# Performance work log

Hardware: AMD Instinct MI355X
Metric: run time of the kernel (lower is better)

The kernel has to match this reference:

```python
import jax, jax.numpy as jnp
import numpy as np

B, R, S, L, H, A, TD = 4, 8, 8, 256, 768, 256, 100


def setup_inputs() -> dict:
    key = jax.random.key(0)
    ks = iter(jax.random.split(key, 64))
    n = lambda *s: jax.random.normal(next(ks), s, jnp.float32)
    p = lambda *s: jax.random.normal(next(ks), s, jnp.float32) * 0.02
    inp = {
        'X': n(B, L, H),
        'X_mean': n(B, H),
        'mask': jnp.ones((B, L), jnp.float32),
        'sk': jax.random.randint(next(ks), (B, R, S, 2), 0, L, dtype=jnp.int32),
        'sk_mask': jnp.ones((B, R, S), jnp.float32),
        'semantic_rel_emb': n(R, H),
        'transe_rel_emb': n(R, TD),
    }
    # 4 EntityExtractors (reconstructed as two H->1 linears producing start/end logits)
    for pref in ('fh', 'bt', 'ft', 'bh'):
        inp[pref + '_ws'] = p(H); inp[pref + '_bs'] = p()
        inp[pref + '_we'] = p(H); inp[pref + '_be'] = p()
    # 2 RelationAttentions (fwd: rel_dim=H, bwd: rel_dim=TD)
    for pref, rd in (('fra', H), ('bra', TD)):
        inp[pref + '_Wx'] = p(H, A);  inp[pref + '_bx'] = p(A)
        inp[pref + '_Wr'] = p(rd, A); inp[pref + '_br'] = p(A)
        inp[pref + '_Wg'] = p(H, A);  inp[pref + '_bg'] = p(A)
        inp[pref + '_V'] = p(A);      inp[pref + '_bv'] = p()
    # 2 FuseExtractors
    for pref in ('ffe', 'bfe'):
        inp[pref + '_Ws'] = p(H, H); inp[pref + '_bs'] = p(H)
        inp[pref + '_Wx'] = p(H, H); inp[pref + '_bx'] = p(H)
    return inp


def _entity(h, ws, bs, we, be):
    # EntityExtractor: start/end logits over last (H) axis
    return jnp.einsum('...h,h->...', h, ws) + bs, jnp.einsum('...h,h->...', h, we) + be


def _rel_attn(X, rel, g, Wx, bx, Wr, br, Wg, bg, V, bv):
    wx = X @ Wx + bx          # (B,L,A)
    wr = rel @ Wr + br        # (R,A)
    wg = g @ Wg + bg          # (B,A)
    z = jnp.tanh(wx[:, None, :, :] + wr[None, :, None, :] + wg[:, None, None, :])  # (B,R,L,A)
    e = jnp.einsum('brla,a->brl', z, V) + bv
    a = jax.nn.softmax(e, axis=-1)                       # (B,R,L)
    c = jnp.einsum('brl,blh->brh', a, X)                 # (B,R,H)
    return c, a


def _sk_to_embeddings(sk, sk_mask, X):
    # vectorized span-endpoint gather + average (replaces B*R*S python loop)
    b_idx = jnp.arange(X.shape[0])[:, None, None]        # (B,1,1)
    emb = (X[b_idx, sk[..., 0]] + X[b_idx, sk[..., 1]]) * 0.5   # (B,R,S,H)
    return sk_mask[..., None] * emb


def _fuse(X, c, sk_embs, sk_mask, Ws, bs, Wx, bx):
    w_x = X @ Wx + bx                                    # (B,L,H)
    w_sk = (sk_embs @ Ws + bs) * sk_mask[..., None]      # (B,R,S,H)
    # h_ijk = Ws*sk + Wx*x_i + c_j + x_i  -> (B,R,S,L,H)
    return (w_sk[:, :, :, None, :] + w_x[:, None, None, :, :]
            + c[:, :, None, None, :] + X[:, None, None, :, :])


def reference(X, X_mean, mask, sk, sk_mask, semantic_rel_emb, transe_rel_emb,
              fh_ws, fh_bs, fh_we, fh_be, bt_ws, bt_bs, bt_we, bt_be,
              ft_ws, ft_bs, ft_we, ft_be, bh_ws, bh_bs, bh_we, bh_be,
              fra_Wx, fra_bx, fra_Wr, fra_br, fra_Wg, fra_bg, fra_V, fra_bv,
              bra_Wx, bra_bx, bra_Wr, bra_br, bra_Wg, bra_bg, bra_V, bra_bv,
              ffe_Ws, ffe_bs, ffe_Wx, ffe_bx, bfe_Ws, bfe_bs, bfe_Wx, bfe_bx):
    fh_s, fh_e = _entity(X, fh_ws, fh_bs, fh_we, fh_be)      # (B,L)
    bt_s, bt_e = _entity(X, bt_ws, bt_bs, bt_we, bt_be)      # (B,L)
    fwd_c, _ = _rel_attn(X, semantic_rel_emb, X_mean,
                         fra_Wx, fra_bx, fra_Wr, fra_br, fra_Wg, fra_bg, fra_V, fra_bv)
    bwd_c, _ = _rel_attn(X, transe_rel_emb, X_mean,
                         bra_Wx, bra_bx, bra_Wr, bra_br, bra_Wg, bra_bg, bra_V, bra_bv)
    sk_embs = _sk_to_embeddings(sk, sk_mask, X)              # (B,R,S,H)
    fwd_hijk = _fuse(X, fwd_c, sk_embs, sk_mask, ffe_Ws, ffe_bs, ffe_Wx, ffe_bx)
    bwd_hijk = _fuse(X, bwd_c, sk_embs, sk_mask, bfe_Ws, bfe_bs, bfe_Wx, bfe_bx)
    ft_s, ft_e = _entity(fwd_hijk, ft_ws, ft_bs, ft_we, ft_be)  # (B,R,S,L)
    bh_s, bh_e = _entity(bwd_hijk, bh_ws, bh_bs, bh_we, bh_be)  # (B,R,S,L)
    return (fh_s, fh_e, bt_s, bt_e, ft_s, ft_e, bh_s, bh_e)
```

## Files before the change

### kernel.cpp

```cpp
#include <hip/hip_runtime.h>
#include <hip/hip_bf16.h>

#define NB 4
#define NR 8
#define NS 8
#define NL 256
#define NH 768
#define NA 256
#define NTD 100

#define WX_F 0
#define WX_B (WX_F + NB*NL*NA)
#define WR_F (WX_B + NB*NL*NA)
#define WR_B (WR_F + NR*NA)
#define WG_F (WR_B + NR*NA)
#define WG_B (WG_F + NB*NA)
#define C_F  (WG_B + NB*NA)
#define C_B  (C_F + NB*NR*NH)
#define QV   (C_B + NB*NR*NH)
#define SCAL (QV + 8*NH)
#define DXL  (SCAL + 8)
#define XB   (DXL + 4*NB*NL)
#define WT   (XB + (NB*NL*NH)/2)

#define O_FT_S 4096
#define O_FT_E 69632
#define O_BH_S 135168
#define O_BH_E 200704

typedef __attribute__((ext_vector_type(8))) short short8;
typedef __attribute__((ext_vector_type(4))) float f32x4;

struct bh4 { __hip_bfloat16 a, b, c, d; };

__device__ __forceinline__ float tanh_fast(float x) {
    x = fminf(15.f, fmaxf(-15.f, x));
    float t = __expf(2.f * x);
    return (t - 1.f) / (t + 1.f);
}

__device__ __forceinline__ float wave_reduce(float v) {
    #pragma unroll
    for (int off = 32; off > 0; off >>= 1) v += __shfl_down(v, off);
    return v;
}

__global__ void __launch_bounds__(512) k_setup(const float* __restrict__ X,
                      const float* __restrict__ fra_Wx, const float* __restrict__ bra_Wx,
                      const float* __restrict__ sem, const float* __restrict__ transe,
                      const float* __restrict__ X_mean,
                      const float* __restrict__ fra_Wr, const float* __restrict__ fra_br,
                      const float* __restrict__ fra_Wg, const float* __restrict__ fra_bg,
                      const float* __restrict__ bra_Wr, const float* __restrict__ bra_br,
                      const float* __restrict__ bra_Wg, const float* __restrict__ bra_bg,
                      const float* __restrict__ ffe_Ws, const float* __restrict__ ffe_bs,
                      const float* __restrict__ ffe_Wx, const float* __restrict__ ffe_bx,
                      const float* __restrict__ bfe_Ws, const float* __restrict__ bfe_bs,
                      const float* __restrict__ bfe_Wx, const float* __restrict__ bfe_bx,
                      const float* __restrict__ ft_ws, const float* __restrict__ ft_we,
                      const float* __restrict__ bh_ws, const float* __restrict__ bh_we,
                      float* __restrict__ ws) {
    __shared__ float smem[2112];
    const int bid = blockIdx.x, tid = threadIdx.x;

    if (bid < 384) {
        __hip_bfloat16* xb = (__hip_bfloat16*)(ws + XB);
        const int i0 = bid*2048 + tid*4;
        const float4 v = *(const float4*)(X + i0);
        bh4 o = { __float2bfloat16(v.x), __float2bfloat16(v.y),
                  __float2bfloat16(v.z), __float2bfloat16(v.w) };
        *(bh4*)(xb + i0) = o;
    } else if (bid < 576) {
        __hip_bfloat16* wt = (__hip_bfloat16*)(ws + WT);
        const int t2 = bid - 384;
        const int mt = t2 / 96;
        const int half = tid >> 8, tid2 = tid & 255;
        const int tile = (t2 % 96)*2 + half;
        const int h0 = (tile >> 3) * 32, c0 = (tile & 7) * 32;
        const float* W = mt ? bra_Wx : fra_Wx;
        float (*sh)[33] = (float(*)[33])(smem + half*1056);
        const int r = tid2 >> 5, c = tid2 & 31;
        #pragma unroll
        for (int i = 0; i < 4; ++i)
            sh[r + 8*i][c] = W[(size_t)(h0 + r + 8*i)*NA + c0 + c];
        __syncthreads();
        const int cw = tid2 >> 5, hw = tid2 & 31;
        #pragma unroll
        for (int i = 0; i < 4; ++i)
            wt[(size_t)(mt*NA + c0 + cw + 8*i)*NH + h0 + hw] = __float2bfloat16(sh[hw][cw + 8*i]);
    } else if (bid < 600) {
        float* sh = smem;
        float* red2 = smem + 768;
        const int q = bid - 576;
        const float* s; const float* W; const float* bias; float* out; int K;
        if (q < 8)       { s = sem + q*NH;         W = fra_Wr; bias = fra_br; out = ws + WR_F + q*NA;      K = NH;  }
        else if (q < 16) { s = transe + (q-8)*NTD; W = bra_Wr; bias = bra_br; out = ws + WR_B + (q-8)*NA;  K = NTD; }
        else if (q < 20) { s = X_mean + (q-16)*NH; W = fra_Wg; bias = fra_bg; out = ws + WG_F + (q-16)*NA; K = NH;  }
        else             { s = X_mean + (q-20)*NH; W = bra_Wg; bias = bra_bg; out = ws + WG_B + (q-20)*NA; K = NH;  }
        for (int j = tid; j < K; j += 512) sh[j] = s[j];
        __syncthreads();
        const int half = tid >> 8, col = tid & 255;
        const int khalf = (K/2) & ~15;
        const int k0 = half ? khalf : 0, k1 = half ? K : khalf;
        const float* Wc = W + col;
        float acc = 0.f;
        int k = k0;
        for (; k + 16 <= k1; k += 16) {
            float wb[16];
            #pragma unroll
            for (int i = 0; i < 16; ++i) wb[i] = Wc[(size_t)(k+i)*NA];
            #pragma unroll
            for (int i = 0; i < 16; ++i) acc += sh[k+i] * wb[i];
        }
        for (; k < k1; ++k) acc += sh[k] * Wc[(size_t)k*NA];
        red2[half*256 + col] = acc;
        __syncthreads();
        if (half == 0) out[col] = red2[col] + red2[256 + col] + bias[col];
    } else if (bid < 608) {
        float* red2 = smem;
        const int q = bid - 600;
        const float* a; const float* b2;
        switch (q) {
            case 0: a = ffe_bs; b2 = ft_ws; break;
            case 1: a = ffe_bs; b2 = ft_we; break;
            case 2: a = ffe_bx; b2 = ft_ws; break;
            case 3: a = ffe_bx; b2 = ft_we; break;
            case 4: a = bfe_bs; b2 = bh_ws; break;
            case 5: a = bfe_bs; b2 = bh_we; break;
            case 6: a = bfe_bx; b2 = bh_ws; break;
            default: a = bfe_bx; b2 = bh_we; break;
        }
        float p = a[tid]*b2[tid];
        if (tid < 256) p += a[tid+512]*b2[tid+512];
        red2[tid] = p; __syncthreads();
        for (int s2 = 256; s2 > 0; s2 >>= 1) { if (tid < s2) red2[tid] += red2[tid + s2]; __syncthreads(); }
        if (tid == 0) ws[SCAL + q] = red2[0];
    } else {
        const int idx = bid - 608;
        const int mi = idx / 96;
        const int row = (idx % 96)*8 + (tid >> 6);
        const int lane = tid & 63;
        const float* M; const float* v0; const float* v1; bool self;
        switch (mi) {
            case 0: M = ffe_Ws; v0 = ft_ws; v1 = ft_we; self = false; break;
            case 1: M = bfe_Ws; v0 = bh_ws; v1 = bh_we; self = false; break;
            case 2: M = ffe_Wx; v0 = ft_ws; v1 = ft_we; self = true;  break;
            default: M = bfe_Wx; v0 = bh_ws; v1 = bh_we; self = true; break;
        }
        const float4* mr4 = (const float4*)(M + (size_t)row*NH);
        const float4* va4 = (const float4*)v0;
        const float4* vb4 = (const float4*)v1;
        float a0 = 0.f, a1 = 0.f;
        #pragma unroll
        for (int i = 0; i < 3; ++i) {
            const float4 m4 = mr4[lane + 64*i];
            const float4 x4 = va4[lane + 64*i];
            const float4 y4 = vb4[lane + 64*i];
            a0 += m4.x*x4.x + m4.y*x4.y + m4.z*x4.z + m4.w*x4.w;
            a1 += m4.x*y4.x + m4.y*y4.y + m4.z*y4.z + m4.w*y4.w;
        }
        a0 = wave_reduce(a0); a1 = wave_reduce(a1);
        if (lane == 0) {
            ws[QV + (mi*2 + 0)*NH + row] = a0 + (self ? v0[row] : 0.f);
            ws[QV + (mi*2 + 1)*NH + row] = a1 + (self ? v1[row] : 0.f);
        }
    }
}

__global__ void __launch_bounds__(256) k_wx(const float* __restrict__ fra_bx,
                                            const float* __restrict__ bra_bx,
                                            float* __restrict__ ws) {
    const __hip_bfloat16* xb = (const __hip_bfloat16*)(ws + XB);
    const __hip_bfloat16* wt = (const __hip_bfloat16*)(ws + WT);
    const int bid = blockIdx.x, tid = threadIdx.x;
    const int fb = bid >> 8;
    const int rt = (bid & 255) >> 2, cg = bid & 3;
    const int wv = tid >> 6, lane = tid & 63;
    const int m0 = rt * 16, c0 = cg * 64 + wv * 16;
    const int r16 = lane & 15, koff = (lane >> 4) * 8;

    const short8* ap = (const short8*)(xb + (size_t)(m0 + r16)*NH + koff);
    const short8* bp = (const short8*)(wt + (size_t)(fb*NA + c0 + r16)*NH + koff);

    f32x4 acc = {0.f, 0.f, 0.f, 0.f};
    #pragma unroll
    for (int ks = 0; ks < 24; ks += 4) {
        short8 a0 = ap[(ks+0)*4], b0 = bp[(ks+0)*4];
        short8 a1 = ap[(ks+1)*4], b1 = bp[(ks+1)*4];
        short8 a2 = ap[(ks+2)*4], b2 = bp[(ks+2)*4];
        short8 a3 = ap[(ks+3)*4], b3 = bp[(ks+3)*4];
        acc = __builtin_amdgcn_mfma_f32_16x16x32_bf16(a0, b0, acc, 0, 0, 0);
        acc = __builtin_amdgcn_mfma_f32_16x16x32_bf16(a1, b1, acc, 0, 0, 0);
        acc = __builtin_amdgcn_mfma_f32_16x16x32_bf16(a2, b2, acc, 0, 0, 0);
        acc = __builtin_amdgcn_mfma_f32_16x16x32_bf16(a3, b3, acc, 0, 0, 0);
    }
    const float* bia = fb ? bra_bx : fra_bx;
    float* outp = ws + (fb ? WX_B : WX_F);
    const int col = c0 + r16;
    const float bb = bia[col];
    const int rbase = m0 + (lane >> 4) * 4;
    #pragma unroll
    for (int j = 0; j < 4; ++j)
        outp[(size_t)(rbase + j)*NA + col] = acc[j] + bb;
}

__global__ void __launch_bounds__(512) k_attn_dxl(const float* __restrict__ X,
                       const float* __restrict__ fra_V, const float* __restrict__ fra_bv,
                       const float* __restrict__ bra_V, const float* __restrict__ bra_bv,
                       const float* __restrict__ fh_ws, const float* __restrict__ fh_bs,
                       const float* __restrict__ fh_we, const float* __restrict__ fh_be,
                       const float* __restrict__ bt_ws, const float* __restrict__ bt_bs,
                       const float* __restrict__ bt_we, const float* __restrict__ bt_be,
                       float* __restrict__ ws, float* __restrict__ out) {
    __shared__ float smem[1536];
    const int bid = blockIdx.x, tid = threadIdx.x;

    if (bid < 64) {
        float* wa_s = smem;
        float* v_s  = smem + 256;
        float* red  = smem + 512;
        float* part = smem + 768;
        float* a_s  = smem + 1024;
        const int fb = bid >> 5, b = (bid >> 3) & 3, r = bid & 7;
        const int l = tid & 255, half = tid >> 8;

        const float* wr = ws + (fb ? WR_B : WR_F) + r*NA;
        const float* wg = ws + (fb ? WG_B : WG_F) + b*NA;
        const float* V  = fb ? bra_V : fra_V;
        const float  bv = fb ? bra_bv[0] : fra_bv[0];
        const float* wxp = ws + (fb ? WX_B : WX_F);

        if (tid < 256) { wa_s[tid] = wr[tid] + wg[tid]; v_s[tid] = V[tid]; }
        __syncthreads();

        const float4* wxrow = (const float4*)(wxp + (size_t)(b*NL + l)*NA + half*128);
        float acc = 0.f;
        for (int a0 = 0; a0 < 32; a0 += 8) {
            float4 wb[8];
            #pragma unroll
            for (int i = 0; i < 8; ++i) wb[i] = wxrow[a0 + i];
            #pragma unroll
            for (int i = 0; i < 8; ++i) {
                const int a = half*128 + (a0 + i)*4;
                acc += tanh_fast(wb[i].x + wa_s[a+0]) * v_s[a+0];
                acc += tanh_fast(wb[i].y + wa_s[a+1]) * v_s[a+1];
                acc += tanh_fast(wb[i].z + wa_s[a+2]) * v_s[a+2];
                acc += tanh_fast(wb[i].w + wa_s[a+3]) * v_s[a+3];
            }
        }
        if (half) part[l] = acc;
        __syncthreads();

        float e = 0.f;
        if (!half) e = acc + part[l] + bv;
        if (tid < 256) red[tid] = e;
        __syncthreads();
        for (int s2 = 128; s2 > 0; s2 >>= 1) { if (tid < s2) red[tid] = fmaxf(red[tid], red[tid+s2]); __syncthreads(); }
        const float mx = red[0];
        __syncthreads();
        float p = 0.f;
        if (tid < 256) { p = __expf(e - mx); red[tid] = p; }
        __syncthreads();
        for (int s2 = 128; s2 > 0; s2 >>= 1) { if (tid < s2) red[tid] += red[tid+s2]; __syncthreads(); }
        if (tid < 256) a_s[tid] = p / red[0];
        __syncthreads();

        const float* Xb = X + (size_t)b*NL*NH;
        float* cc = ws + (fb ? C_B : C_F) + (size_t)(b*NR + r)*NH;
        for (int h = tid; h < NH; h += 512) {
            const float* Xp = Xb + h;
            float c = 0.f;
            for (int l0 = 0; l0 < NL; l0 += 8) {
                float xb_[8];
                #pragma unroll
                for (int i = 0; i < 8; ++i) xb_[i] = Xp[(size_t)(l0+i)*NH];
                #pragma unroll
                for (int i = 0; i < 8; ++i) c += a_s[l0+i] * xb_[i];
            }
            cc[h] = c;
        }
    } else {
        float* xr = smem;
        const int idx = bid - 64;
        const int m0 = idx * 2;
        const int g = tid >> 6, lane = tid & 63;
        const int row = g >> 2, w = g & 3;
        const int m = m0 + row;

        if (tid < 384) ((float4*)xr)[tid] = ((const float4*)(X + (size_t)m0*NH))[tid];
        __syncthreads();

        const float* v0; const float* v1; float add0, add1; float* o0; float* o1;
        if (w == 0)      { v0 = fh_ws; add0 = fh_bs[0]; o0 = out;        v1 = fh_we; add1 = fh_be[0]; o1 = out + 1024; }
        else if (w == 1) { v0 = bt_ws; add0 = bt_bs[0]; o0 = out + 2048; v1 = bt_we; add1 = bt_be[0]; o1 = out + 3072; }
        else if (w == 2) { v0 = ws + QV + 4*NH; add0 = ws[SCAL+2]; o0 = ws + DXL;
                           v1 = ws + QV + 5*NH; add1 = ws[SCAL+3]; o1 = ws + DXL + 1024; }
        else             { v0 = ws + QV + 6*NH; add0 = ws[SCAL+6]; o0 = ws + DXL + 2048;
                           v1 = ws + QV + 7*NH; add1 = ws[SCAL+7]; o1 = ws + DXL + 3072; }

        const float4* xr4 = (const float4*)(xr + row*NH);
        const float4* v04 = (const float4*)v0;
        const float4* v14 = (const float4*)v1;
        float a0 = 0.f, a1 = 0.f;
        #pragma unroll
        for (int i = 0; i < 3; ++i) {
            const float4 x4 = xr4[lane + 64*i];
            const float4 p4 = v04[lane + 64*i];
            const float4 q4 = v14[lane + 64*i];
            a0 += x4.x*p4.x + x4.y*p4.y + x4.z*p4.z + x4.w*p4.w;
            a1 += x4.x*q4.x + x4.y*q4.y + x4.z*q4.z + x4.w*q4.w;
        }
        a0 = wave_reduce(a0); a1 = wave_reduce(a1);
        if (lane == 0) { o0[m] = a0 + add0; o1[m] = a1 + add1; }
    }
}

__global__ void __launch_bounds__(256) k_skf(const float* __restrict__ X, const int* __restrict__ sk,
                     const float* __restrict__ sk_mask,
                     const float* __restrict__ ft_ws, const float* __restrict__ ft_bs,
                     const float* __restrict__ ft_we, const float* __restrict__ ft_be,
                     const float* __restrict__ bh_ws, const float* __restrict__ bh_bs,
                     const float* __restrict__ bh_we, const float* __restrict__ bh_be,
                     const float* __restrict__ ws, float* __restrict__ out) {
    __shared__ float avg[NH];
    __shared__ float d1_s[4], d3_s[4];
    const int brs = blockIdx.x;
    const int tid = threadIdx.x, w = tid >> 6, lane = tid & 63;
    const int b = brs >> 6, br = brs >> 3;
    const int i0 = sk[brs*2], i1 = sk[brs*2 + 1];
    const float mk = sk_mask[brs];

    if (tid < 192) {
        const float4 x0 = ((const float4*)(X + (size_t)(b*NL + i0)*NH))[tid];
        const float4 x1 = ((const float4*)(X + (size_t)(b*NL + i1)*NH))[tid];
        float4 o; o.x = 0.5f*(x0.x+x1.x); o.y = 0.5f*(x0.y+x1.y);
        o.z = 0.5f*(x0.z+x1.z); o.w = 0.5f*(x0.w+x1.w);
        ((float4*)avg)[tid] = o;
    }
    __syncthreads();

    const float4* q4 = (const float4*)(ws + QV + w*NH);
    const float4* av4 = (const float4*)avg;
    const float4* c4 = (const float4*)(ws + ((w < 2) ? C_F : C_B) + (size_t)br*NH);
    const float* v = (w == 0) ? ft_ws : (w == 1) ? ft_we : (w == 2) ? bh_ws : bh_we;
    const float4* vv4 = (const float4*)v;
    float acc = 0.f, d = 0.f;
    #pragma unroll
    for (int i = 0; i < 3; ++i) {
        const float4 a4 = av4[lane + 64*i];
        const float4 b4 = q4[lane + 64*i];
        const float4 e4 = c4[lane + 64*i];
        const float4 f4 = vv4[lane + 64*i];
        acc += a4.x*b4.x + a4.y*b4.y + a4.z*b4.z + a4.w*b4.w;
        d   += e4.x*f4.x + e4.y*f4.y + e4.z*f4.z + e4.w*f4.w;
    }
    acc = wave_reduce(acc); d = wave_reduce(d);
    if (lane == 0) {
        const float bsdot = ws[SCAL + ((w < 2) ? w : (w + 2))];
        d1_s[w] = mk*mk*acc + mk*bsdot;
        d3_s[w] = d;
    }
    __syncthreads();

    const int l = tid, m = b*NL + l, o = brs*NL + l;
    out[O_FT_S + o] = d1_s[0] + ws[DXL + 0*1024 + m] + d3_s[0] + ft_bs[0];
    out[O_FT_E + o] = d1_s[1] + ws[DXL + 1*1024 + m] + d3_s[1] + ft_be[0];
    out[O_BH_S + o] = d1_s[2] + ws[DXL + 2*1024 + m] + d3_s[2] + bh_bs[0];
    out[O_BH_E + o] = d1_s[3] + ws[DXL + 3*1024 + m] + d3_s[3] + bh_be[0];
}

extern "C" void kernel_launch(void* const* d_in, const int* in_sizes, int n_in,
                              void* d_out, int out_size, void* d_ws, size_t ws_size,
                              hipStream_t stream) {
    const float* X        = (const float*)d_in[0];
    const float* X_mean   = (const float*)d_in[1];
    const int*   sk       = (const int*)d_in[3];
    const float* sk_mask  = (const float*)d_in[4];
    const float* sem      = (const float*)d_in[5];
    const float* transe   = (const float*)d_in[6];
    const float* fh_ws = (const float*)d_in[7],  *fh_bs = (const float*)d_in[8];
    const float* fh_we = (const float*)d_in[9],  *fh_be = (const float*)d_in[10];
    const float* bt_ws = (const float*)d_in[11], *bt_bs = (const float*)d_in[12];
    const float* bt_we = (const float*)d_in[13], *bt_be = (const float*)d_in[14];
    const float* ft_ws = (const float*)d_in[15], *ft_bs = (const float*)d_in[16];
    const float* ft_we = (const float*)d_in[17], *ft_be = (const float*)d_in[18];
    const float* bh_ws = (const float*)d_in[19], *bh_bs = (const float*)d_in[20];
    const float* bh_we = (const float*)d_in[21], *bh_be = (const float*)d_in[22];
    const float* fra_Wx = (const float*)d_in[23], *fra_bx = (const float*)d_in[24];
    const float* fra_Wr = (const float*)d_in[25], *fra_br = (const float*)d_in[26];
    const float* fra_Wg = (const float*)d_in[27], *fra_bg = (const float*)d_in[28];
    const float* fra_V  = (const float*)d_in[29], *fra_bv = (const float*)d_in[30];
    const float* bra_Wx = (const float*)d_in[31], *bra_bx = (const float*)d_in[32];
    const float* bra_Wr = (const float*)d_in[33], *bra_br = (const float*)d_in[34];
    const float* bra_Wg = (const float*)d_in[35], *bra_bg = (const float*)d_in[36];
    const float* bra_V  = (const float*)d_in[37], *bra_bv = (const float*)d_in[38];
    const float* ffe_Ws = (const float*)d_in[39], *ffe_bs = (const float*)d_in[40];
    const float* ffe_Wx = (const float*)d_in[41], *ffe_bx = (const float*)d_in[42];
    const float* bfe_Ws = (const float*)d_in[43], *bfe_bs = (const float*)d_in[44];
    const float* bfe_Wx = (const float*)d_in[45], *bfe_bx = (const float*)d_in[46];

    float* out = (float*)d_out;
    float* ws  = (float*)d_ws;

    k_setup<<<dim3(992), dim3(512), 0, stream>>>(X, fra_Wx, bra_Wx, sem, transe, X_mean,
        fra_Wr, fra_br, fra_Wg, fra_bg, bra_Wr, bra_br, bra_Wg, bra_bg,
        ffe_Ws, ffe_bs, ffe_Wx, ffe_bx, bfe_Ws, bfe_bs, bfe_Wx, bfe_bx,
        ft_ws, ft_we, bh_ws, bh_we, ws);

    k_wx<<<dim3(512), dim3(256), 0, stream>>>(fra_bx, bra_bx, ws);

    k_attn_dxl<<<dim3(576), dim3(512), 0, stream>>>(X, fra_V, fra_bv, bra_V, bra_bv,
        fh_ws, fh_bs, fh_we, fh_be, bt_ws, bt_bs, bt_we, bt_be, ws, out);

    k_skf<<<dim3(256), dim3(256), 0, stream>>>(X, sk, sk_mask,
        ft_ws, ft_bs, ft_we, ft_be, bh_ws, bh_bs, bh_we, bh_be, ws, out);
}
```

Baseline: 251.2 us.

## Compute attention context with bf16 MFMA over transposed X, split attention kernel

The attention kernel now writes softmax weights as bf16, zero-padded to 16 rows, into a workspace buffer. A new k_ctx kernel computes the context vectors c = a·X with 16x16x32 bf16 MFMA, using a bf16 transposed copy of X that extra setup blocks produce. This replaces the old per-thread strided fp32 loop over L. The row-dot products over X move into their own k_dxl launch with one block per row. The change trades fp32 precision in the context sum and two extra launches for matrix-core throughput and coalesced access.

```diff
diff --git a/kernel.cpp b/kernel.cpp
--- a/kernel.cpp
+++ b/kernel.cpp
@@ -20,8 +20,10 @@
 #define QV   (C_B + NB*NR*NH)
 #define SCAL (QV + 8*NH)
 #define DXL  (SCAL + 8)
-#define XB   (DXL + 4*NB*NL)
+#define ATT16 (DXL + 4*NB*NL)
+#define XB   (ATT16 + 16384)
 #define WT   (XB + (NB*NL*NH)/2)
+#define XT   (WT + (2*NA*NH)/2)
 
 #define O_FT_S 4096
 #define O_FT_E 69632
@@ -84,14 +86,29 @@
         for (int i = 0; i < 4; ++i)
             sh[r + 8*i][c] = W[(size_t)(h0 + r + 8*i)*NA + c0 + c];
         __syncthreads();
-        const int cw = tid2 >> 5, hw = tid2 & 31;
         #pragma unroll
         for (int i = 0; i < 4; ++i)
-            wt[(size_t)(mt*NA + c0 + cw + 8*i)*NH + h0 + hw] = __float2bfloat16(sh[hw][cw + 8*i]);
-    } else if (bid < 600) {
+            wt[(size_t)(mt*NA + c0 + r + 8*i)*NH + h0 + c] = __float2bfloat16(sh[c][r + 8*i]);
+    } else if (bid < 960) {
+        __hip_bfloat16* xt = (__hip_bfloat16*)(ws + XT);
+        const int t2 = bid - 576;
+        const int half = tid >> 8, tid2 = tid & 255;
+        const int tile = t2*2 + half;
+        const int b = tile / 192, trem = tile % 192;
+        const int h0 = (trem >> 3) * 32, l0 = (trem & 7) * 32;
+        float (*sh)[33] = (float(*)[33])(smem + half*1056);
+        const int r = tid2 >> 5, c = tid2 & 31;
+        #pragma unroll
+        for (int i = 0; i < 4; ++i)
+            sh[r + 8*i][c] = X[(size_t)(b*NL + l0 + r + 8*i)*NH + h0 + c];
+        __syncthreads();
+        #pragma unroll
+        for (int i = 0; i < 4; ++i)
+            xt[(size_t)(b*NH + h0 + r + 8*i)*NL + l0 + c] = __float2bfloat16(sh[c][r + 8*i]);
+    } else if (bid < 984) {
         float* sh = smem;
         float* red2 = smem + 768;
-        const int q = bid - 576;
+        const int q = bid - 960;
         const float* s; const float* W; const float* bias; float* out; int K;
         if (q < 8)       { s = sem + q*NH;         W = fra_Wr; bias = fra_br; out = ws + WR_F + q*NA;      K = NH;  }
         else if (q < 16) { s = transe + (q-8)*NTD; W = bra_Wr; bias = bra_br; out = ws + WR_B + (q-8)*NA;  K = NTD; }
@@ -116,9 +133,9 @@
         red2[half*256 + col] = acc;
         __syncthreads();
         if (half == 0) out[col] = red2[col] + red2[256 + col] + bias[col];
-    } else if (bid < 608) {
+    } else if (bid < 992) {
         float* red2 = smem;
-        const int q = bid - 600;
+        const int q = bid - 984;
         const float* a; const float* b2;
         switch (q) {
             case 0: a = ffe_bs; b2 = ft_ws; break;
@@ -136,7 +153,7 @@
         for (int s2 = 256; s2 > 0; s2 >>= 1) { if (tid < s2) red2[tid] += red2[tid + s2]; __syncthreads(); }
         if (tid == 0) ws[SCAL + q] = red2[0];
     } else {
-        const int idx = bid - 608;
+        const int idx = bid - 992;
         const int mi = idx / 96;
         const int row = (idx % 96)*8 + (tid >> 6);
         const int lane = tid & 63;
@@ -204,115 +221,125 @@
         outp[(size_t)(rbase + j)*NA + col] = acc[j] + bb;
 }
 
-__global__ void __launch_bounds__(512) k_attn_dxl(const float* __restrict__ X,
-                       const float* __restrict__ fra_V, const float* __restrict__ fra_bv,
+__global__ void __launch_bounds__(512) k_attn(const float* __restrict__ fra_V, const float* __restrict__ fra_bv,
                        const float* __restrict__ bra_V, const float* __restrict__ bra_bv,
-                       const float* __restrict__ fh_ws, const float* __restrict__ fh_bs,
-                       const float* __restrict__ fh_we, const float* __restrict__ fh_be,
-                       const float* __restrict__ bt_ws, const float* __restrict__ bt_bs,
-                       const float* __restrict__ bt_we, const float* __restrict__ bt_be,
-                       float* __restrict__ ws, float* __restrict__ out) {
-    __shared__ float smem[1536];
+                       float* __restrict__ ws) {
+    __shared__ float wa_s[NA], v_s[NA], red[NL], part[NL];
     const int bid = blockIdx.x, tid = threadIdx.x;
-
-    if (bid < 64) {
-        float* wa_s = smem;
-        float* v_s  = smem + 256;
-        float* red  = smem + 512;
-        float* part = smem + 768;
-        float* a_s  = smem + 1024;
-        const int fb = bid >> 5, b = (bid >> 3) & 3, r = bid & 7;
-        const int l = tid & 255, half = tid >> 8;
-
-        const float* wr = ws + (fb ? WR_B : WR_F) + r*NA;
-        const float* wg = ws + (fb ? WG_B : WG_F) + b*NA;
-        const float* V  = fb ? bra_V : fra_V;
-        const float  bv = fb ? bra_bv[0] : fra_bv[0];
-        const float* wxp = ws + (fb ? WX_B : WX_F);
-
-        if (tid < 256) { wa_s[tid] = wr[tid] + wg[tid]; v_s[tid] = V[tid]; }
-        __syncthreads();
-
-        const float4* wxrow = (const float4*)(wxp + (size_t)(b*NL + l)*NA + half*128);
-        float acc = 0.f;
-        for (int a0 = 0; a0 < 32; a0 += 8) {
-            float4 wb[8];
-            #pragma unroll
-            for (int i = 0; i < 8; ++i) wb[i] = wxrow[a0 + i];
-            #pragma unroll
-            for (int i = 0; i < 8; ++i) {
-                const int a = half*128 + (a0 + i)*4;
-                acc += tanh_fast(wb[i].x + wa_s[a+0]) * v_s[a+0];
-                acc += tanh_fast(wb[i].y + wa_s[a+1]) * v_s[a+1];
-                acc += tanh_fast(wb[i].z + wa_s[a+2]) * v_s[a+2];
-                acc += tanh_fast(wb[i].w + wa_s[a+3]) * v_s[a+3];
-            }
-        }
-        if (half) part[l] = acc;
-        __syncthreads();
-
-        float e = 0.f;
-        if (!half) e = acc + part[l] + bv;
-        if (tid < 256) red[tid] = e;
-        __syncthreads();
-        for (int s2 = 128; s2 > 0; s2 >>= 1) { if (tid < s2) red[tid] = fmaxf(red[tid], red[tid+s2]); __syncthreads(); }
-        const float mx = red[0];
-        __syncthreads();
-        float p = 0.f;
-        if (tid < 256) { p = __expf(e - mx); red[tid] = p; }
-        __syncthreads();
-        for (int s2 = 128; s2 > 0; s2 >>= 1) { if (tid < s2) red[tid] += red[tid+s2]; __syncthreads(); }
-        if (tid < 256) a_s[tid] = p / red[0];
-        __syncthreads();
-
-        const float* Xb = X + (size_t)b*NL*NH;
-        float* cc = ws + (fb ? C_B : C_F) + (size_t)(b*NR + r)*NH;
-        for (int h = tid; h < NH; h += 512) {
-            const float* Xp = Xb + h;
-            float c = 0.f;
-            for (int l0 = 0; l0 < NL; l0 += 8) {
-                float xb_[8];
-                #pragma unroll
-                for (int i = 0; i < 8; ++i) xb_[i] = Xp[(size_t)(l0+i)*NH];
-                #pragma unroll
-                for (int i = 0; i < 8; ++i) c += a_s[l0+i] * xb_[i];
-            }
-            cc[h] = c;
-        }
-    } else {
-        float* xr = smem;
-        const int idx = bid - 64;
-        const int m0 = idx * 2;
-        const int g = tid >> 6, lane = tid & 63;
-        const int row = g >> 2, w = g & 3;
-        const int m = m0 + row;
-
-        if (tid < 384) ((float4*)xr)[tid] = ((const float4*)(X + (size_t)m0*NH))[tid];
-        __syncthreads();
-
-        const float* v0; const float* v1; float add0, add1; float* o0; float* o1;
-        if (w == 0)      { v0 = fh_ws; add0 = fh_bs[0]; o0 = out;        v1 = fh_we; add1 = fh_be[0]; o1 = out + 1024; }
-        else if (w == 1) { v0 = bt_ws; add0 = bt_bs[0]; o0 = out + 2048; v1 = bt_we; add1 = bt_be[0]; o1 = out + 3072; }
-        else if (w == 2) { v0 = ws + QV + 4*NH; add0 = ws[SCAL+2]; o0 = ws + DXL;
-                           v1 = ws + QV + 5*NH; add1 = ws[SCAL+3]; o1 = ws + DXL + 1024; }
-        else             { v0 = ws + QV + 6*NH; add0 = ws[SCAL+6]; o0 = ws + DXL + 2048;
-                           v1 = ws + QV + 7*NH; add1 = ws[SCAL+7]; o1 = ws + DXL + 3072; }
-
-        const float4* xr4 = (const float4*)(xr + row*NH);
-        const float4* v04 = (const float4*)v0;
-        const float4* v14 = (const float4*)v1;
-        float a0 = 0.f, a1 = 0.f;
-        #pragma unroll
-        for (int i = 0; i < 3; ++i) {
-            const float4 x4 = xr4[lane + 64*i];
-            const float4 p4 = v04[lane + 64*i];
-            const float4 q4 = v14[lane + 64*i];
-            a0 += x4.x*p4.x + x4.y*p4.y + x4.z*p4.z + x4.w*p4.w;
-            a1 += x4.x*q4.x + x4.y*q4.y + x4.z*q4.z + x4.w*q4.w;
-        }
-        a0 = wave_reduce(a0); a1 = wave_reduce(a1);
-        if (lane == 0) { o0[m] = a0 + add0; o1[m] = a1 + add1; }
-    }
+    const int fb = bid >> 5, b = (bid >> 3) & 3, r = bid & 7;
+    const int l = tid & 255, half = tid >> 8;
+
+    const float* wr = ws + (fb ? WR_B : WR_F) + r*NA;
+    const float* wg = ws + (fb ? WG_B : WG_F) + b*NA;
+    const float* V  = fb ? bra_V : fra_V;
+    const float  bv = fb ? bra_bv[0] : fra_bv[0];
+    const float* wxp = ws + (fb ? WX_B : WX_F);
+
+    if (tid < 256) { wa_s[tid] = wr[tid] + wg[tid]; v_s[tid] = V[tid]; }
+    __syncthreads();
+
+    const float4* wxrow = (const float4*)(wxp + (size_t)(b*NL + l)*NA + half*128);
+    float acc = 0.f;
+    for (int a0 = 0; a0 < 32; a0 += 8) {
+        float4 wb[8];
+        #pragma unroll
+        for (int i = 0; i < 8; ++i) wb[i] = wxrow[a0 + i];
+        #pragma unroll
+        for (int i = 0; i < 8; ++i) {
+            const int a = half*128 + (a0 + i)*4;
+            acc += tanh_fast(wb[i].x + wa_s[a+0]) * v_s[a+0];
+            acc += tanh_fast(wb[i].y + wa_s[a+1]) * v_s[a+1];
+            acc += tanh_fast(wb[i].z + wa_s[a+2]) * v_s[a+2];
+            acc += tanh_fast(wb[i].w + wa_s[a+3]) * v_s[a+3];
+        }
+    }
+    if (half) part[l] = acc;
+    __syncthreads();
+
+    float e = 0.f;
+    if (!half) e = acc + part[l] + bv;
+    if (tid < 256) red[tid] = e;
+    __syncthreads();
+    for (int s2 = 128; s2 > 0; s2 >>= 1) { if (tid < s2) red[tid] = fmaxf(red[tid], red[tid+s2]); __syncthreads(); }
+    const float mx = red[0];
+    __syncthreads();
+    float p = 0.f;
+    if (tid < 256) { p = __expf(e - mx); red[tid] = p; }
+    __syncthreads();
+    for (int s2 = 128; s2 > 0; s2 >>= 1) { if (tid < s2) red[tid] += red[tid+s2]; __syncthreads(); }
+    if (tid < 256) {
+        __hip_bfloat16* att = (__hip_bfloat16*)(ws + ATT16);
+        const int g = fb*NB + b;
+        att[(size_t)(g*16 + r)*NL + tid]     = __float2bfloat16(p / red[0]);
+        att[(size_t)(g*16 + 8 + r)*NL + tid] = __float2bfloat16(0.f);
+    }
+}
+
+__global__ void __launch_bounds__(256) k_ctx(float* __restrict__ ws) {
+    const __hip_bfloat16* att = (const __hip_bfloat16*)(ws + ATT16);
+    const __hip_bfloat16* xt  = (const __hip_bfloat16*)(ws + XT);
+    const int bid = blockIdx.x, tid = threadIdx.x;
+    const int g = bid / 12, hc = bid % 12;
+    const int fb = g >> 2, b = g & 3;
+    const int wv = tid >> 6, lane = tid & 63;
+    const int h0 = hc*64 + wv*16;
+    const int r16 = lane & 15, khi = lane >> 4;
+
+    const short8* ap = (const short8*)(att + (size_t)(g*16 + r16)*NL) + khi;
+    const short8* bp = (const short8*)(xt + (size_t)(b*NH + h0 + r16)*NL) + khi;
+
+    f32x4 acc = {0.f, 0.f, 0.f, 0.f};
+    #pragma unroll
+    for (int ks = 0; ks < 8; ++ks) {
+        short8 af = ap[ks*4];
+        short8 bf = bp[ks*4];
+        acc = __builtin_amdgcn_mfma_f32_16x16x32_bf16(af, bf, acc, 0, 0, 0);
+    }
+    float* cc = ws + (fb ? C_B : C_F) + (size_t)b*NR*NH;
+    const int col = h0 + r16;
+    const int rbase = khi * 4;
+    #pragma unroll
+    for (int j = 0; j < 4; ++j) {
+        const int r = rbase + j;
+        if (r < 8) cc[(size_t)r*NH + col] = acc[j];
+    }
+}
+
+__global__ void __launch_bounds__(256) k_dxl(const float* __restrict__ X,
+                      const float* __restrict__ fh_ws, const float* __restrict__ fh_bs,
+                      const float* __restrict__ fh_we, const float* __restrict__ fh_be,
+                      const float* __restrict__ bt_ws, const float* __restrict__ bt_bs,
+                      const float* __restrict__ bt_we, const float* __restrict__ bt_be,
+                      float* __restrict__ ws, float* __restrict__ out) {
+    __shared__ float xr[NH];
+    const int m = blockIdx.x;
+    const int tid = threadIdx.x, w = tid >> 6, lane = tid & 63;
+
+    if (tid < 192) ((float4*)xr)[tid] = ((const float4*)(X + (size_t)m*NH))[tid];
+    __syncthreads();
+
+    const float* v0; const float* v1; float add0, add1; float* o0; float* o1;
+    if (w == 0)      { v0 = fh_ws; add0 = fh_bs[0]; o0 = out;        v1 = fh_we; add1 = fh_be[0]; o1 = out + 1024; }
+    else if (w == 1) { v0 = bt_ws; add0 = bt_bs[0]; o0 = out + 2048; v1 = bt_we; add1 = bt_be[0]; o1 = out + 3072; }
+    else if (w == 2) { v0 = ws + QV + 4*NH; add0 = ws[SCAL+2]; o0 = ws + DXL;
+                       v1 = ws + QV + 5*NH; add1 = ws[SCAL+3]; o1 = ws + DXL + 1024; }
+    else             { v0 = ws + QV + 6*NH; add0 = ws[SCAL+6]; o0 = ws + DXL + 2048;
+                       v1 = ws + QV + 7*NH; add1 = ws[SCAL+7]; o1 = ws + DXL + 3072; }
+
+    const float4* xr4 = (const float4*)xr;
+    const float4* v04 = (const float4*)v0;
+    const float4* v14 = (const float4*)v1;
+    float a0 = 0.f, a1 = 0.f;
+    #pragma unroll
+    for (int i = 0; i < 3; ++i) {
+        const float4 x4 = xr4[lane + 64*i];
+        const float4 p4 = v04[lane + 64*i];
+        const float4 q4 = v14[lane + 64*i];
+        a0 += x4.x*p4.x + x4.y*p4.y + x4.z*p4.z + x4.w*p4.w;
+        a1 += x4.x*q4.x + x4.y*q4.y + x4.z*q4.z + x4.w*q4.w;
+    }
+    a0 = wave_reduce(a0); a1 = wave_reduce(a1);
+    if (lane == 0) { o0[m] = a0 + add0; o1[m] = a1 + add1; }
 }
 
 __global__ void __launch_bounds__(256) k_skf(const float* __restrict__ X, const int* __restrict__ sk,
@@ -402,15 +429,19 @@
     float* out = (float*)d_out;
     float* ws  = (float*)d_ws;
 
-    k_setup<<<dim3(992), dim3(512), 0, stream>>>(X, fra_Wx, bra_Wx, sem, transe, X_mean,
+    k_setup<<<dim3(1376), dim3(512), 0, stream>>>(X, fra_Wx, bra_Wx, sem, transe, X_mean,
         fra_Wr, fra_br, fra_Wg, fra_bg, bra_Wr, bra_br, bra_Wg, bra_bg,
         ffe_Ws, ffe_bs, ffe_Wx, ffe_bx, bfe_Ws, bfe_bs, bfe_Wx, bfe_bx,
         ft_ws, ft_we, bh_ws, bh_we, ws);
 
     k_wx<<<dim3(512), dim3(256), 0, stream>>>(fra_bx, bra_bx, ws);
 
-    k_attn_dxl<<<dim3(576), dim3(512), 0, stream>>>(X, fra_V, fra_bv, bra_V, bra_bv,
-        fh_ws, fh_bs, fh_we, fh_be, bt_ws, bt_bs, bt_we, bt_be, ws, out);
+    k_attn<<<dim3(64), dim3(512), 0, stream>>>(fra_V, fra_bv, bra_V, bra_bv, ws);
+
+    k_ctx<<<dim3(96), dim3(256), 0, stream>>>(ws);
+
+    k_dxl<<<dim3(1024), dim3(256), 0, stream>>>(X, fh_ws, fh_bs, fh_we, fh_be,
+        bt_ws, bt_bs, bt_we, bt_be, ws, out);
 
     k_skf<<<dim3(256), dim3(256), 0, stream>>>(X, sk, sk_mask,
         ft_ws, ft_bs, ft_we, ft_be, bh_ws, bh_bs, bh_we, bh_be, ws, out);
```

New measurement: 205.1 us. 18.4% less time.
